# Kernel optimization log

Hardware: AMD Instinct MI355X
Metric: run time of the kernel (lower is better)

Reference implementation:

```python
import jax, jax.numpy as jnp
import numpy as np


def _cos_map(N):
    # DCT-II basis: weight[n, x] = cos(n*(x+0.5)/N*pi)*sqrt(2/N), row 0 scaled by 1/sqrt(2)
    pos = (jnp.arange(N, dtype=jnp.float32) + 0.5) / N
    n = jnp.arange(N, dtype=jnp.float32)[:, None]
    w = jnp.cos(n * pos[None, :] * jnp.pi) * np.sqrt(2.0 / N)
    return w.at[0].multiply(1.0 / np.sqrt(2.0))


def _dct3(x, cT, cH, cW):
    # x: [B,C,T,H,W]; matmul(x, cos.T) along each axis
    x = jnp.einsum('bcthw,Ww->bcthW', x, cW)
    x = jnp.einsum('bcthw,Hh->bctHw', x, cH)
    x = jnp.einsum('bcthw,Tt->bcThw', x, cT)
    return x


def _idct3(x, cT, cH, cW):
    # matmul(x, cos) along each axis
    x = jnp.einsum('bcthw,wW->bcthW', x, cW)
    x = jnp.einsum('bcthw,hH->bctHw', x, cH)
    x = jnp.einsum('bcthw,tT->bcThw', x, cT)
    return x


def setup_inputs() -> dict:
    key = jax.random.key(0)
    ks = jax.random.split(key, 12)
    B, C, T, H, W = 2, 96, 16, 64, 64
    hd = 96
    s = 0.02
    return {
        'x': jax.random.normal(ks[0], (B, C, T, H, W), jnp.float32),
        'freq_embed': jax.random.normal(ks[1], (T, H, W, hd), jnp.float32),
        'dwconv_w': jax.random.normal(ks[2], (hd, 1, 3, 3, 3), jnp.float32) * s,
        'dwconv_b': jnp.zeros((hd,), jnp.float32),
        'linear_w': jax.random.normal(ks[3], (2 * hd, hd), jnp.float32) * s,
        'linear_b': jnp.zeros((2 * hd,), jnp.float32),
        'v0_w': jax.random.normal(ks[4], (hd, hd), jnp.float32) * s,
        'v0_b': jnp.zeros((hd,), jnp.float32),
        'tok_w': jax.random.normal(ks[5], (hd, hd), jnp.float32) * s,
        'tok_b': jnp.zeros((hd,), jnp.float32),
        'c': jnp.ones((1,), jnp.float32),
        'alpha': jnp.full((1,), 0.1, jnp.float32),
        'ln_g': jnp.ones((hd,), jnp.float32),
        'ln_b': jnp.zeros((hd,), jnp.float32),
        'out_w': jax.random.normal(ks[6], (hd, hd), jnp.float32) * s,
        'out_b': jnp.zeros((hd,), jnp.float32),
    }


def reference(x, freq_embed, dwconv_w, dwconv_b, linear_w, linear_b, v0_w, v0_b,
              tok_w, tok_b, c, alpha, ln_g, ln_b, out_w, out_b):
    B, C, T, H, W = x.shape
    hd = C
    # depthwise 3x3x3 conv
    y = jax.lax.conv_general_dilated(
        x, dwconv_w, (1, 1, 1), [(1, 1)] * 3,
        dimension_numbers=('NCDHW', 'OIDHW', 'NCDHW'), feature_group_count=hd)
    y = y + dwconv_b[None, :, None, None, None]
    yl = jnp.moveaxis(y, 1, -1)                     # [B,T,H,W,C]
    lin = yl @ linear_w.T + linear_b                # [B,T,H,W,2C]
    xg, z = jnp.split(lin, 2, axis=-1)
    v0 = xg @ v0_w.T + v0_b
    xc = jnp.moveaxis(xg, -1, 1)                    # [B,C,T,H,W]
    v0c = jnp.moveaxis(v0, -1, 1)
    cT, cH, cW = _cos_map(T), _cos_map(H), _cos_map(W)
    x_u0 = _dct3(xc, cT, cH, cW)
    x_v0 = _dct3(v0c, cT, cH, cW)
    # tau from freq_embed (exact GELU, as torch default)
    tau = jax.nn.gelu(freq_embed @ tok_w.T + tok_b, approximate=False)  # [T,H,W,C]
    tau = jnp.moveaxis(tau, -1, 0)[None]            # [1,C,T,H,W] broadcasts over B
    c_tau = c[0] * tau
    damping = jnp.exp(-alpha[0] / 2 * tau)
    spec = damping * (jnp.cos(c_tau) * x_u0 +
                      jnp.sin(c_tau) / (c[0] + 1e-8) * (x_v0 + alpha[0] / 2 * x_u0))
    xf = _idct3(spec, cT, cH, cW)
    xf = jnp.moveaxis(xf, 1, -1)                    # [B,T,H,W,C]
    mu = xf.mean(-1, keepdims=True)
    var = ((xf - mu) ** 2).mean(-1, keepdims=True)
    xf = (xf - mu) / jnp.sqrt(var + 1e-5) * ln_g + ln_b
    xf = xf * jax.nn.silu(z)                        # elementwise gate
    out = xf @ out_w.T + out_b
    return jnp.moveaxis(out, -1, 1)                 # [B,C,T,H,W]
```

## Files before the change

kernel.cpp:

```cpp
#include <hip/hip_runtime.h>
#include <math.h>

#define THW 65536
#define HW  4096
#define C96 96
#ifndef M_PI
#define M_PI 3.14159265358979323846
#endif

__global__ __launch_bounds__(256) void init_basis_k(float* __restrict__ b64,
                                                    float* __restrict__ b64T,
                                                    float* __restrict__ b16) {
  int tid = threadIdx.x;
  for (int i = tid; i < 4096; i += 256) {
    int n = i >> 6, x = i & 63;
    double s = sqrt(2.0 / 64.0) * (n == 0 ? sqrt(0.5) : 1.0);
    float v = (float)(cos((double)n * ((double)x + 0.5) * M_PI / 64.0) * s);
    b64[i] = v;
    b64T[x * 64 + n] = v;
  }
  {
    int n = tid >> 4, x = tid & 15;
    double s = sqrt(2.0 / 16.0) * (n == 0 ? sqrt(0.5) : 1.0);
    b16[tid & 255] = (float)(cos((double)n * ((double)x + 0.5) * M_PI / 16.0) * s);
  }
}

struct R3 { float a, b, c; };

#define LOADR(dst, row) { int rr_ = (row); int o_ = rr_ * 64 + lane; \
    dst.a = pmv[o_]; dst.b = pcv[o_]; dst.c = ppv[o_]; }

#define OUTROW(A, B, Cc, row) { \
    float P0, P1, P2; \
    P0 = w27[0]  * A.a;          P1 = w27[1]  * A.a;          P2 = w27[2]  * A.a; \
    P0 = fmaf(w27[3],  B.a, P0); P1 = fmaf(w27[4],  B.a, P1); P2 = fmaf(w27[5],  B.a, P2); \
    P0 = fmaf(w27[6],  Cc.a, P0); P1 = fmaf(w27[7],  Cc.a, P1); P2 = fmaf(w27[8],  Cc.a, P2); \
    P0 = fmaf(w27[9],  A.b, P0); P1 = fmaf(w27[10], A.b, P1); P2 = fmaf(w27[11], A.b, P2); \
    P0 = fmaf(w27[12], B.b, P0); P1 = fmaf(w27[13], B.b, P1); P2 = fmaf(w27[14], B.b, P2); \
    P0 = fmaf(w27[15], Cc.b, P0); P1 = fmaf(w27[16], Cc.b, P1); P2 = fmaf(w27[17], Cc.b, P2); \
    P0 = fmaf(w27[18], A.c, P0); P1 = fmaf(w27[19], A.c, P1); P2 = fmaf(w27[20], A.c, P2); \
    P0 = fmaf(w27[21], B.c, P0); P1 = fmaf(w27[22], B.c, P1); P2 = fmaf(w27[23], B.c, P2); \
    P0 = fmaf(w27[24], Cc.c, P0); P1 = fmaf(w27[25], Cc.c, P1); P2 = fmaf(w27[26], Cc.c, P2); \
    float lft = __shfl_up(P0, 1);  if (lane == 0)  lft = 0.f; \
    float rgt = __shfl_down(P2, 1); if (lane == 63) rgt = 0.f; \
    yp[(row) * 64] = bv + lft + P1 + rgt; }

__global__ __launch_bounds__(256) void dwconv_k(const float* __restrict__ x,
    const float* __restrict__ wv, const float* __restrict__ bias,
    float* __restrict__ y) {
  int lane = threadIdx.x & 63;
  int wvi  = threadIdx.x >> 6;
  int bc   = blockIdx.x;
  int t    = blockIdx.y * 4 + wvi;
  int h0   = blockIdx.z * 32;
  int c    = bc % C96;

  const float* pcv = x + (size_t)bc * THW + (size_t)t * HW;
  const float* pmv = (t > 0)  ? pcv - HW : pcv;
  const float* ppv = (t < 15) ? pcv + HW : pcv;

  float w27[27];
#pragma unroll
  for (int i = 0; i < 27; ++i) w27[i] = wv[c * 27 + i];
  if (t == 0) {
#pragma unroll
    for (int i = 0; i < 9; ++i) w27[i] = 0.f;
  }
  if (t == 15) {
#pragma unroll
    for (int i = 0; i < 9; ++i) w27[18 + i] = 0.f;
  }
  float bv = bias[c];
  float* yp = y + (size_t)bc * THW + (size_t)t * HW + lane;

  R3 s0, s1, s2, s3, n0, n1;
  if (h0 > 0) { LOADR(s0, h0 - 1) } else { s0.a = s0.b = s0.c = 0.f; }
  LOADR(s1, h0)
  LOADR(s2, h0 + 1)
  LOADR(s3, h0 + 2)
#pragma unroll
  for (int p = 0; p < 14; ++p) {
    int h = h0 + 2 * p;
    LOADR(n0, h + 3)
    LOADR(n1, h + 4)
    OUTROW(s0, s1, s2, h)
    OUTROW(s1, s2, s3, h + 1)
    s0 = s2; s1 = s3; s2 = n0; s3 = n1;
  }
  {
    int h = h0 + 28;
    LOADR(n0, h + 3)
    if (h0 == 0) { LOADR(n1, h + 4) }
    else { n1.a = n1.b = n1.c = 0.f; }
    OUTROW(s0, s1, s2, h)
    OUTROW(s1, s2, s3, h + 1)
    s0 = s2; s1 = s3; s2 = n0; s3 = n1;
  }
  {
    int h = h0 + 30;
    OUTROW(s0, s1, s2, h)
    OUTROW(s1, s2, s3, h + 1)
  }
}
#undef LOADR
#undef OUTROW

__global__ __launch_bounds__(256) void feT_k(const float* __restrict__ fe,
                                             float* __restrict__ feT) {
  __shared__ float t[96 * 65];
  int tid = threadIdx.x;
  int tok0 = blockIdx.x * 64;
  const float* p = fe + (size_t)tok0 * 96;
  for (int i = tid; i < 6144; i += 256) {
    int tok = i / 96;
    int ch = i - tok * 96;
    t[ch * 65 + tok] = p[i];
  }
  __syncthreads();
  for (int i = tid; i < 6144; i += 256) {
    int ch = i >> 6, tok = i & 63;
    feT[(size_t)ch * THW + tok0 + tok] = t[ch * 65 + tok];
  }
}

#define FMA4(A, WV) \
  A.x = fmaf(WV, v.x, A.x); A.y = fmaf(WV, v.y, A.y); \
  A.z = fmaf(WV, v.z, A.z); A.w = fmaf(WV, v.w, A.w);

#define WPAD 104
#define BK32 32

template <int EPI>
__global__ __launch_bounds__(512) void gemm96_k(
    const float* __restrict__ In, const float* __restrict__ W,
    const float* __restrict__ bias, float* __restrict__ Out,
    float* __restrict__ Out2, const float* __restrict__ zg,
    const float* __restrict__ lnG, const float* __restrict__ lnB,
    const float* __restrict__ scal_c, const float* __restrict__ scal_a,
    int N, size_t inStride, size_t outStride) {
  __shared__ float Wt[96 * WPAD];
  __shared__ float buf[BK32 * 256];
  int tid = threadIdx.x;
  int wvi = tid >> 6, ln = tid & 63;
  for (int i = tid; i < 2304; i += 512) {
    int k4 = i / 96, co = i - k4 * 96;
    float4 w4 = *(const float4*)(W + co * 96 + k4 * 4);
    int k = k4 * 4;
    Wt[(k + 0) * WPAD + co] = w4.x;
    Wt[(k + 1) * WPAD + co] = w4.y;
    Wt[(k + 2) * WPAD + co] = w4.z;
    Wt[(k + 3) * WPAD + co] = w4.w;
  }
  int n0 = blockIdx.x * 256 + ln * 4;
  int co0 = wvi * 12;
  const float* ipb = In + blockIdx.y * inStride + blockIdx.x * 256 + ln * 4;
  const float* zpb = (EPI == 2) ? (zg + blockIdx.y * inStride + blockIdx.x * 256 + ln * 4)
                                : nullptr;

  float4 mu4, rs4;
  if (EPI == 2) {
    float4 sum = make_float4(0.f, 0.f, 0.f, 0.f);
    float4 sq  = make_float4(0.f, 0.f, 0.f, 0.f);
#pragma unroll 8
    for (int ci = 0; ci < 96; ++ci) {
      float4 t = *(const float4*)(ipb + (size_t)ci * N);
      sum.x += t.x; sum.y += t.y; sum.z += t.z; sum.w += t.w;
      sq.x = fmaf(t.x, t.x, sq.x); sq.y = fmaf(t.y, t.y, sq.y);
      sq.z = fmaf(t.z, t.z, sq.z); sq.w = fmaf(t.w, t.w, sq.w);
    }
    const float r96 = 1.0f / 96.0f;
    mu4.x = sum.x * r96; mu4.y = sum.y * r96; mu4.z = sum.z * r96; mu4.w = sum.w * r96;
    rs4.x = rsqrtf(fmaxf(sq.x * r96 - mu4.x * mu4.x, 0.f) + 1e-5f);
    rs4.y = rsqrtf(fmaxf(sq.y * r96 - mu4.y * mu4.y, 0.f) + 1e-5f);
    rs4.z = rsqrtf(fmaxf(sq.z * r96 - mu4.z * mu4.z, 0.f) + 1e-5f);
    rs4.w = rsqrtf(fmaxf(sq.w * r96 - mu4.w * mu4.w, 0.f) + 1e-5f);
  }

  float4 acc[12];
#pragma unroll
  for (int j = 0; j < 12; ++j) {
    float bj = bias[co0 + j];
    acc[j] = make_float4(bj, bj, bj, bj);
  }

#pragma unroll 1
  for (int kb = 0; kb < 3; ++kb) {
#pragma unroll
    for (int i = 0; i < 4; ++i) {
      int r = i * 8 + wvi;
      int k = kb * BK32 + r;
      float4 v4 = *(const float4*)(ipb + (size_t)k * N);
      if (EPI == 2) {
        float4 zz = *(const float4*)(zpb + (size_t)k * N);
        float lgk = lnG[k], lbk = lnB[k];
        float gx = zz.x * __builtin_amdgcn_rcpf(1.0f + __expf(-zz.x));
        float gy = zz.y * __builtin_amdgcn_rcpf(1.0f + __expf(-zz.y));
        float gz = zz.z * __builtin_amdgcn_rcpf(1.0f + __expf(-zz.z));
        float gw = zz.w * __builtin_amdgcn_rcpf(1.0f + __expf(-zz.w));
        v4.x = fmaf((v4.x - mu4.x) * rs4.x, lgk, lbk) * gx;
        v4.y = fmaf((v4.y - mu4.y) * rs4.y, lgk, lbk) * gy;
        v4.z = fmaf((v4.z - mu4.z) * rs4.z, lgk, lbk) * gz;
        v4.w = fmaf((v4.w - mu4.w) * rs4.w, lgk, lbk) * gw;
      }
      *(float4*)&buf[r * 256 + ln * 4] = v4;
    }
    __syncthreads();
#pragma unroll 8
    for (int kk = 0; kk < BK32; ++kk) {
      int k = kb * BK32 + kk;
      float4 v = *(const float4*)&buf[kk * 256 + ln * 4];
      const float4* wr = (const float4*)&Wt[k * WPAD + co0];
#pragma unroll
      for (int j = 0; j < 3; ++j) {
        float4 wvv = wr[j];
        FMA4(acc[4 * j + 0], wvv.x);
        FMA4(acc[4 * j + 1], wvv.y);
        FMA4(acc[4 * j + 2], wvv.z);
        FMA4(acc[4 * j + 3], wvv.w);
      }
    }
    __syncthreads();
  }

  if (EPI == 1) {
    float cv = scal_c[0], al = scal_a[0];
    float rc = 1.0f / (cv + 1e-8f);
#define TAUMAP(T, AA, BB) { \
    float tau = 0.5f * (T) * (1.0f + erff((T) * 0.70710678118654752f)); \
    float ct = cv * tau; \
    float damp = __expf(-0.5f * al * tau); \
    float sc = __sinf(ct), cc = __cosf(ct); \
    AA = damp * (cc + sc * al * 0.5f * rc); BB = damp * sc * rc; }
#pragma unroll 2
    for (int j = 0; j < 12; ++j) {
      float4 a4, b4;
      TAUMAP(acc[j].x, a4.x, b4.x);
      TAUMAP(acc[j].y, a4.y, b4.y);
      TAUMAP(acc[j].z, a4.z, b4.z);
      TAUMAP(acc[j].w, a4.w, b4.w);
      *(float4*)(Out  + (size_t)(co0 + j) * N + n0) = a4;
      *(float4*)(Out2 + (size_t)(co0 + j) * N + n0) = b4;
    }
#undef TAUMAP
  } else {
    float* op = Out + blockIdx.y * outStride + n0;
#pragma unroll
    for (int j = 0; j < 12; ++j)
      *(float4*)(op + (size_t)(co0 + j) * N) = acc[j];
  }
}

__global__ __launch_bounds__(256) void wh_k(const float* __restrict__ in,
    float* __restrict__ out, const float* __restrict__ basis) {
  __shared__ float XT[64 * 68];
  __shared__ float Yb[64 * 68];
  __shared__ float Bs[64 * 68];
  int tid = threadIdx.x;
  const float* ip = in + (size_t)blockIdx.x * HW;
  float* op = out + (size_t)blockIdx.x * HW;
  for (int i = tid; i < 1024; i += 256) {
    int r = i >> 4, c4 = i & 15;
    float4 v = *(const float4*)(basis + r * 64 + c4 * 4);
    *(float4*)&Bs[r * 68 + c4 * 4] = v;
  }
  for (int i = tid; i < 1024; i += 256) {
    int h = i >> 4, w4 = i & 15;
    float4 v = *(const float4*)(ip + h * 64 + w4 * 4);
    int w = w4 * 4;
    XT[(w + 0) * 68 + h] = v.x;
    XT[(w + 1) * 68 + h] = v.y;
    XT[(w + 2) * 68 + h] = v.z;
    XT[(w + 3) * 68 + h] = v.w;
  }
  __syncthreads();
  int nb = tid & 15, rb = tid >> 4;
  int n0 = nb * 4, r0 = rb * 4;
  {
    float4 a0 = make_float4(0.f, 0.f, 0.f, 0.f), a1 = a0, a2 = a0, a3 = a0;
#pragma unroll 8
    for (int w = 0; w < 64; ++w) {
      float4 xv = *(const float4*)&XT[w * 68 + r0];
      float4 bv = *(const float4*)&Bs[w * 68 + n0];
      a0.x = fmaf(xv.x, bv.x, a0.x); a0.y = fmaf(xv.x, bv.y, a0.y);
      a0.z = fmaf(xv.x, bv.z, a0.z); a0.w = fmaf(xv.x, bv.w, a0.w);
      a1.x = fmaf(xv.y, bv.x, a1.x); a1.y = fmaf(xv.y, bv.y, a1.y);
      a1.z = fmaf(xv.y, bv.z, a1.z); a1.w = fmaf(xv.y, bv.w, a1.w);
      a2.x = fmaf(xv.z, bv.x, a2.x); a2.y = fmaf(xv.z, bv.y, a2.y);
      a2.z = fmaf(xv.z, bv.z, a2.z); a2.w = fmaf(xv.z, bv.w, a2.w);
      a3.x = fmaf(xv.w, bv.x, a3.x); a3.y = fmaf(xv.w, bv.y, a3.y);
      a3.z = fmaf(xv.w, bv.z, a3.z); a3.w = fmaf(xv.w, bv.w, a3.w);
    }
    *(float4*)&Yb[(r0 + 0) * 68 + n0] = a0;
    *(float4*)&Yb[(r0 + 1) * 68 + n0] = a1;
    *(float4*)&Yb[(r0 + 2) * 68 + n0] = a2;
    *(float4*)&Yb[(r0 + 3) * 68 + n0] = a3;
  }
  __syncthreads();
  {
    float4 a0 = make_float4(0.f, 0.f, 0.f, 0.f), a1 = a0, a2 = a0, a3 = a0;
#pragma unroll 8
    for (int h = 0; h < 64; ++h) {
      float4 bv = *(const float4*)&Bs[h * 68 + r0];
      float4 yv = *(const float4*)&Yb[h * 68 + n0];
      a0.x = fmaf(bv.x, yv.x, a0.x); a0.y = fmaf(bv.x, yv.y, a0.y);
      a0.z = fmaf(bv.x, yv.z, a0.z); a0.w = fmaf(bv.x, yv.w, a0.w);
      a1.x = fmaf(bv.y, yv.x, a1.x); a1.y = fmaf(bv.y, yv.y, a1.y);
      a1.z = fmaf(bv.y, yv.z, a1.z); a1.w = fmaf(bv.y, yv.w, a1.w);
      a2.x = fmaf(bv.z, yv.x, a2.x); a2.y = fmaf(bv.z, yv.y, a2.y);
      a2.z = fmaf(bv.z, yv.z, a2.z); a2.w = fmaf(bv.z, yv.w, a2.w);
      a3.x = fmaf(bv.w, yv.x, a3.x); a3.y = fmaf(bv.w, yv.y, a3.y);
      a3.z = fmaf(bv.w, yv.z, a3.z); a3.w = fmaf(bv.w, yv.w, a3.w);
    }
    *(float4*)&op[(r0 + 0) * 64 + n0] = a0;
    *(float4*)&op[(r0 + 1) * 64 + n0] = a1;
    *(float4*)&op[(r0 + 2) * 64 + n0] = a2;
    *(float4*)&op[(r0 + 3) * 64 + n0] = a3;
  }
}

__global__ __launch_bounds__(256) void tspec_k(const float* __restrict__ U0,
    const float* __restrict__ V0, const float* __restrict__ A,
    const float* __restrict__ Bc, const float* __restrict__ b16,
    float* __restrict__ out) {
  __shared__ float bs[256];
  int tid = threadIdx.x;
  bs[tid] = b16[tid];
  __syncthreads();
  int hw = blockIdx.x * 256 + tid;
  int c = blockIdx.y, b = blockIdx.z;
  size_t base = ((size_t)(b * C96 + c) * 16) * HW + hw;
  int cbase = c * THW + hw;
  float ua[16], va[16];
  {
    float u[16];
#pragma unroll
    for (int t = 0; t < 16; ++t) u[t] = U0[base + t * HW];
#pragma unroll
    for (int n = 0; n < 16; ++n) {
      float s = 0.0f;
#pragma unroll
      for (int t = 0; t < 16; ++t) s = fmaf(bs[n * 16 + t], u[t], s);
      ua[n] = s;
    }
  }
  {
    float v[16];
#pragma unroll
    for (int t = 0; t < 16; ++t) v[t] = V0[base + t * HW];
#pragma unroll
    for (int n = 0; n < 16; ++n) {
      float s = 0.0f;
#pragma unroll
      for (int t = 0; t < 16; ++t) s = fmaf(bs[n * 16 + t], v[t], s);
      va[n] = s;
    }
  }
  float so[16];
#pragma unroll 4
  for (int n = 0; n < 16; ++n)
    so[n] = A[cbase + n * HW] * ua[n] + Bc[cbase + n * HW] * va[n];
#pragma unroll
  for (int t = 0; t < 16; ++t) {
    float s = 0.0f;
#pragma unroll
    for (int n = 0; n < 16; ++n) s = fmaf(so[n], bs[n * 16 + t], s);
    out[base + t * HW] = s;
  }
}

extern "C" void kernel_launch(void* const* d_in, const int* in_sizes, int n_in,
                              void* d_out, int out_size, void* d_ws, size_t ws_size,
                              hipStream_t stream) {
  const float* x    = (const float*)d_in[0];
  const float* fe   = (const float*)d_in[1];
  const float* dww  = (const float*)d_in[2];
  const float* dwb  = (const float*)d_in[3];
  const float* linW = (const float*)d_in[4];
  const float* linB = (const float*)d_in[5];
  const float* v0W  = (const float*)d_in[6];
  const float* v0B  = (const float*)d_in[7];
  const float* tokW = (const float*)d_in[8];
  const float* tokB = (const float*)d_in[9];
  const float* cS   = (const float*)d_in[10];
  const float* aS   = (const float*)d_in[11];
  const float* lnG  = (const float*)d_in[12];
  const float* lnBp = (const float*)d_in[13];
  const float* outW = (const float*)d_in[14];
  const float* outB = (const float*)d_in[15];
  float* out = (float*)d_out;

  float* w = (float*)d_ws;
  const size_t TEN = (size_t)2 * C96 * THW;
  const size_t BST = (size_t)C96 * THW;
  float* b64    = w;
  float* b64T   = w + 4096;
  float* b16    = w + 8192;
  float* buf_y  = w + 16384;
  float* buf_xg = buf_y + TEN;
  float* buf_z  = buf_xg + TEN;
  float* buf_v0 = buf_z + TEN;
  float* bufA   = buf_v0 + TEN;
  float* bufB   = bufA + BST;
  size_t need = (size_t)(16384 + 4 * TEN + 2 * BST) * sizeof(float);
  if (ws_size < need) return;

  hipLaunchKernelGGL(init_basis_k, dim3(1), dim3(256), 0, stream, b64, b64T, b16);
  hipLaunchKernelGGL(dwconv_k, dim3(192, 4, 2), dim3(256), 0, stream, x, dww, dwb, buf_y);
  hipLaunchKernelGGL((gemm96_k<0>), dim3(256, 2), dim3(512), 0, stream,
                     buf_y, linW, linB, buf_xg, (float*)nullptr, (const float*)nullptr,
                     (const float*)nullptr, (const float*)nullptr,
                     (const float*)nullptr, (const float*)nullptr, THW, BST, BST);
  hipLaunchKernelGGL((gemm96_k<0>), dim3(256, 2), dim3(512), 0, stream,
                     buf_y, linW + 9216, linB + 96, buf_z, (float*)nullptr, (const float*)nullptr,
                     (const float*)nullptr, (const float*)nullptr,
                     (const float*)nullptr, (const float*)nullptr, THW, BST, BST);
  hipLaunchKernelGGL(feT_k, dim3(1024), dim3(256), 0, stream, fe, buf_v0);
  hipLaunchKernelGGL((gemm96_k<1>), dim3(256, 1), dim3(512), 0, stream,
                     buf_v0, tokW, tokB, bufA, bufB, (const float*)nullptr,
                     (const float*)nullptr, (const float*)nullptr,
                     cS, aS, THW, (size_t)0, (size_t)0);
  hipLaunchKernelGGL((gemm96_k<0>), dim3(256, 2), dim3(512), 0, stream,
                     buf_xg, v0W, v0B, buf_v0, (float*)nullptr, (const float*)nullptr,
                     (const float*)nullptr, (const float*)nullptr,
                     (const float*)nullptr, (const float*)nullptr, THW, BST, BST);
  hipLaunchKernelGGL(wh_k, dim3(3072), dim3(256), 0, stream, buf_xg, buf_y, b64T);
  hipLaunchKernelGGL(wh_k, dim3(3072), dim3(256), 0, stream, buf_v0, buf_xg, b64T);
  hipLaunchKernelGGL(tspec_k, dim3(16, 96, 2), dim3(256), 0, stream, buf_y, buf_xg, bufA, bufB, b16, buf_v0);
  hipLaunchKernelGGL(wh_k, dim3(3072), dim3(256), 0, stream, buf_v0, buf_y, b64);
  hipLaunchKernelGGL((gemm96_k<2>), dim3(256, 2), dim3(512), 0, stream,
                     buf_y, outW, outB, out, (float*)nullptr, buf_z,
                     lnG, lnBp, (const float*)nullptr, (const float*)nullptr, THW, BST, BST);
}
```

Before: 570.6 us.

## Read GEMM weights and DCT basis via wave-uniform scalar loads instead of LDS

The 96-channel GEMM no longer stages the transposed weight matrix in shared memory. Each wave reads its 12 output-channel weight rows directly from global memory at a wave-uniform (readfirstlane) address, so the loads can go through the scalar path. The 64x64 W/H DCT kernel is restructured the same way: each lane owns one row and reads basis coefficients with uniform addresses, and only a single padded LDS tile is used for the transpose between the two passes. This cuts LDS footprint and LDS traffic, and may allow more occupancy, at the cost of relying on scalar-cache bandwidth and higher register pressure.

```diff
diff --git a/kernel.cpp b/kernel.cpp
--- a/kernel.cpp
+++ b/kernel.cpp
@@ -128,7 +128,6 @@
   A.x = fmaf(WV, v.x, A.x); A.y = fmaf(WV, v.y, A.y); \
   A.z = fmaf(WV, v.z, A.z); A.w = fmaf(WV, v.w, A.w);
 
-#define WPAD 104
 #define BK32 32
 
 template <int EPI>
@@ -139,21 +138,13 @@
     const float* __restrict__ lnG, const float* __restrict__ lnB,
     const float* __restrict__ scal_c, const float* __restrict__ scal_a,
     int N, size_t inStride, size_t outStride) {
-  __shared__ float Wt[96 * WPAD];
   __shared__ float buf[BK32 * 256];
   int tid = threadIdx.x;
   int wvi = tid >> 6, ln = tid & 63;
-  for (int i = tid; i < 2304; i += 512) {
-    int k4 = i / 96, co = i - k4 * 96;
-    float4 w4 = *(const float4*)(W + co * 96 + k4 * 4);
-    int k = k4 * 4;
-    Wt[(k + 0) * WPAD + co] = w4.x;
-    Wt[(k + 1) * WPAD + co] = w4.y;
-    Wt[(k + 2) * WPAD + co] = w4.z;
-    Wt[(k + 3) * WPAD + co] = w4.w;
-  }
+  int co0 = __builtin_amdgcn_readfirstlane(wvi * 12);
+  const float* Wb = W + co0 * 96;
+
   int n0 = blockIdx.x * 256 + ln * 4;
-  int co0 = wvi * 12;
   const float* ipb = In + blockIdx.y * inStride + blockIdx.x * 256 + ln * 4;
   const float* zpb = (EPI == 2) ? (zg + blockIdx.y * inStride + blockIdx.x * 256 + ln * 4)
                                 : nullptr;
@@ -206,18 +197,21 @@
       *(float4*)&buf[r * 256 + ln * 4] = v4;
     }
     __syncthreads();
-#pragma unroll 8
-    for (int kk = 0; kk < BK32; ++kk) {
-      int k = kb * BK32 + kk;
-      float4 v = *(const float4*)&buf[kk * 256 + ln * 4];
-      const float4* wr = (const float4*)&Wt[k * WPAD + co0];
-#pragma unroll
-      for (int j = 0; j < 3; ++j) {
-        float4 wvv = wr[j];
-        FMA4(acc[4 * j + 0], wvv.x);
-        FMA4(acc[4 * j + 1], wvv.y);
-        FMA4(acc[4 * j + 2], wvv.z);
-        FMA4(acc[4 * j + 3], wvv.w);
+#pragma unroll
+    for (int kk4 = 0; kk4 < 8; ++kk4) {
+      int k0 = kb * BK32 + kk4 * 4;
+      float4 wr[12];
+#pragma unroll
+      for (int j = 0; j < 12; ++j)
+        wr[j] = *(const float4*)(Wb + j * 96 + k0);
+#pragma unroll
+      for (int kkin = 0; kkin < 4; ++kkin) {
+        float4 v = *(const float4*)&buf[(kk4 * 4 + kkin) * 256 + ln * 4];
+#pragma unroll
+        for (int j = 0; j < 12; ++j) {
+          float wvv = ((const float*)&wr[j])[kkin];
+          FMA4(acc[j], wvv);
+        }
       }
     }
     __syncthreads();
@@ -253,70 +247,75 @@
 
 __global__ __launch_bounds__(256) void wh_k(const float* __restrict__ in,
     float* __restrict__ out, const float* __restrict__ basis) {
-  __shared__ float XT[64 * 68];
-  __shared__ float Yb[64 * 68];
-  __shared__ float Bs[64 * 68];
+  __shared__ float Xs[64 * 65];
   int tid = threadIdx.x;
+  int lane = tid & 63;
+  int g0 = __builtin_amdgcn_readfirstlane((tid >> 6) * 16);
   const float* ip = in + (size_t)blockIdx.x * HW;
   float* op = out + (size_t)blockIdx.x * HW;
+
   for (int i = tid; i < 1024; i += 256) {
-    int r = i >> 4, c4 = i & 15;
-    float4 v = *(const float4*)(basis + r * 64 + c4 * 4);
-    *(float4*)&Bs[r * 68 + c4 * 4] = v;
-  }
-  for (int i = tid; i < 1024; i += 256) {
-    int h = i >> 4, w4 = i & 15;
-    float4 v = *(const float4*)(ip + h * 64 + w4 * 4);
-    int w = w4 * 4;
-    XT[(w + 0) * 68 + h] = v.x;
-    XT[(w + 1) * 68 + h] = v.y;
-    XT[(w + 2) * 68 + h] = v.z;
-    XT[(w + 3) * 68 + h] = v.w;
+    int h = i >> 4, w0x = (i & 15) * 4;
+    float4 v = *(const float4*)(ip + h * 64 + w0x);
+    float* d = &Xs[h * 65 + w0x];
+    d[0] = v.x; d[1] = v.y; d[2] = v.z; d[3] = v.w;
   }
   __syncthreads();
-  int nb = tid & 15, rb = tid >> 4;
-  int n0 = nb * 4, r0 = rb * 4;
-  {
-    float4 a0 = make_float4(0.f, 0.f, 0.f, 0.f), a1 = a0, a2 = a0, a3 = a0;
-#pragma unroll 8
+
+  float accp[16];
+#pragma unroll
+  for (int j = 0; j < 16; ++j) accp[j] = 0.f;
+  {
+    const float* xrow = &Xs[lane * 65];
+#pragma unroll 4
     for (int w = 0; w < 64; ++w) {
-      float4 xv = *(const float4*)&XT[w * 68 + r0];
-      float4 bv = *(const float4*)&Bs[w * 68 + n0];
-      a0.x = fmaf(xv.x, bv.x, a0.x); a0.y = fmaf(xv.x, bv.y, a0.y);
-      a0.z = fmaf(xv.x, bv.z, a0.z); a0.w = fmaf(xv.x, bv.w, a0.w);
-      a1.x = fmaf(xv.y, bv.x, a1.x); a1.y = fmaf(xv.y, bv.y, a1.y);
-      a1.z = fmaf(xv.y, bv.z, a1.z); a1.w = fmaf(xv.y, bv.w, a1.w);
-      a2.x = fmaf(xv.z, bv.x, a2.x); a2.y = fmaf(xv.z, bv.y, a2.y);
-      a2.z = fmaf(xv.z, bv.z, a2.z); a2.w = fmaf(xv.z, bv.w, a2.w);
-      a3.x = fmaf(xv.w, bv.x, a3.x); a3.y = fmaf(xv.w, bv.y, a3.y);
-      a3.z = fmaf(xv.w, bv.z, a3.z); a3.w = fmaf(xv.w, bv.w, a3.w);
-    }
-    *(float4*)&Yb[(r0 + 0) * 68 + n0] = a0;
-    *(float4*)&Yb[(r0 + 1) * 68 + n0] = a1;
-    *(float4*)&Yb[(r0 + 2) * 68 + n0] = a2;
-    *(float4*)&Yb[(r0 + 3) * 68 + n0] = a3;
+      float xv = xrow[w];
+      const float* bw = basis + w * 64 + g0;
+      float4 b0 = *(const float4*)(bw);
+      float4 b1 = *(const float4*)(bw + 4);
+      float4 b2 = *(const float4*)(bw + 8);
+      float4 b3 = *(const float4*)(bw + 12);
+      accp[0]  = fmaf(xv, b0.x, accp[0]);  accp[1]  = fmaf(xv, b0.y, accp[1]);
+      accp[2]  = fmaf(xv, b0.z, accp[2]);  accp[3]  = fmaf(xv, b0.w, accp[3]);
+      accp[4]  = fmaf(xv, b1.x, accp[4]);  accp[5]  = fmaf(xv, b1.y, accp[5]);
+      accp[6]  = fmaf(xv, b1.z, accp[6]);  accp[7]  = fmaf(xv, b1.w, accp[7]);
+      accp[8]  = fmaf(xv, b2.x, accp[8]);  accp[9]  = fmaf(xv, b2.y, accp[9]);
+      accp[10] = fmaf(xv, b2.z, accp[10]); accp[11] = fmaf(xv, b2.w, accp[11]);
+      accp[12] = fmaf(xv, b3.x, accp[12]); accp[13] = fmaf(xv, b3.y, accp[13]);
+      accp[14] = fmaf(xv, b3.z, accp[14]); accp[15] = fmaf(xv, b3.w, accp[15]);
+    }
   }
   __syncthreads();
   {
-    float4 a0 = make_float4(0.f, 0.f, 0.f, 0.f), a1 = a0, a2 = a0, a3 = a0;
-#pragma unroll 8
-    for (int h = 0; h < 64; ++h) {
-      float4 bv = *(const float4*)&Bs[h * 68 + r0];
-      float4 yv = *(const float4*)&Yb[h * 68 + n0];
-      a0.x = fmaf(bv.x, yv.x, a0.x); a0.y = fmaf(bv.x, yv.y, a0.y);
-      a0.z = fmaf(bv.x, yv.z, a0.z); a0.w = fmaf(bv.x, yv.w, a0.w);
-      a1.x = fmaf(bv.y, yv.x, a1.x); a1.y = fmaf(bv.y, yv.y, a1.y);
-      a1.z = fmaf(bv.y, yv.z, a1.z); a1.w = fmaf(bv.y, yv.w, a1.w);
-      a2.x = fmaf(bv.z, yv.x, a2.x); a2.y = fmaf(bv.z, yv.y, a2.y);
-      a2.z = fmaf(bv.z, yv.z, a2.z); a2.w = fmaf(bv.z, yv.w, a2.w);
-      a3.x = fmaf(bv.w, yv.x, a3.x); a3.y = fmaf(bv.w, yv.y, a3.y);
-      a3.z = fmaf(bv.w, yv.z, a3.z); a3.w = fmaf(bv.w, yv.w, a3.w);
-    }
-    *(float4*)&op[(r0 + 0) * 64 + n0] = a0;
-    *(float4*)&op[(r0 + 1) * 64 + n0] = a1;
-    *(float4*)&op[(r0 + 2) * 64 + n0] = a2;
-    *(float4*)&op[(r0 + 3) * 64 + n0] = a3;
-  }
+    float* trow = &Xs[lane * 65 + g0];
+#pragma unroll
+    for (int j = 0; j < 16; ++j) trow[j] = accp[j];
+  }
+  __syncthreads();
+
+  float acc2[16];
+#pragma unroll
+  for (int j = 0; j < 16; ++j) acc2[j] = 0.f;
+#pragma unroll 4
+  for (int h = 0; h < 64; ++h) {
+    float tv = Xs[h * 65 + lane];
+    const float* bw = basis + h * 64 + g0;
+    float4 b0 = *(const float4*)(bw);
+    float4 b1 = *(const float4*)(bw + 4);
+    float4 b2 = *(const float4*)(bw + 8);
+    float4 b3 = *(const float4*)(bw + 12);
+    acc2[0]  = fmaf(tv, b0.x, acc2[0]);  acc2[1]  = fmaf(tv, b0.y, acc2[1]);
+    acc2[2]  = fmaf(tv, b0.z, acc2[2]);  acc2[3]  = fmaf(tv, b0.w, acc2[3]);
+    acc2[4]  = fmaf(tv, b1.x, acc2[4]);  acc2[5]  = fmaf(tv, b1.y, acc2[5]);
+    acc2[6]  = fmaf(tv, b1.z, acc2[6]);  acc2[7]  = fmaf(tv, b1.w, acc2[7]);
+    acc2[8]  = fmaf(tv, b2.x, acc2[8]);  acc2[9]  = fmaf(tv, b2.y, acc2[9]);
+    acc2[10] = fmaf(tv, b2.z, acc2[10]); acc2[11] = fmaf(tv, b2.w, acc2[11]);
+    acc2[12] = fmaf(tv, b3.x, acc2[12]); acc2[13] = fmaf(tv, b3.y, acc2[13]);
+    acc2[14] = fmaf(tv, b3.z, acc2[14]); acc2[15] = fmaf(tv, b3.w, acc2[15]);
+  }
+#pragma unroll
+  for (int j = 0; j < 16; ++j)
+    op[(g0 + j) * 64 + lane] = acc2[j];
 }
 
 __global__ __launch_bounds__(256) void tspec_k(const float* __restrict__ U0,
```

Result: slower. 674.4 us (+18.2%).
